# Performance work log

Measured on AMD Instinct MI355X. Metric: run time of the kernel, lower is better.

The kernel has to match this reference:

```python
import jax, jax.numpy as jnp
from jax import lax
import numpy as np

M_FILTERS = 128   # rows of responses D
N_CHANNELS = 1024 # cols of responses D (spectral channels)
BATCH = 4096
N_LAYERS = 17
IMAX = 50


def setup_inputs() -> dict:
    key = jax.random.key(0)
    k1, k2, k3, k4 = jax.random.split(key, 4)
    t1 = jax.random.normal(k1, (BATCH, N_CHANNELS), dtype=jnp.float32)
    t2 = jax.random.normal(k2, (BATCH, N_CHANNELS), dtype=jnp.float32)
    params = jax.random.uniform(k3, (M_FILTERS, N_LAYERS), dtype=jnp.float32)
    responses = jax.random.normal(k4, (M_FILTERS, N_CHANNELS), dtype=jnp.float32)
    return {
        "t1": t1,
        "t2": t2,
        "params": params,
        "thick_min": jnp.float32(0.0),
        "thick_max": jnp.float32(1.0),
        "beta_range": jnp.float32(0.1),
        "responses": responses,
    }


def _coherence_reduce(D0):
    """Faithful vectorized version of the 50-iteration coherence-reduction loop.

    The original per-row Python loop (Ri[i] > Rth branch) only reads row i and
    pre-computed Rth/delta, so it is exactly a masked row update.
    torch.linalg.eig on the symmetric matrices G is replaced by eigh (same
    eigenpairs up to sign/order; order is fixed by the explicit descending sort,
    and only the top-M eigenpairs reach the output D[:M,:]).
    """
    Mr, Nr = D0.shape
    ratio = jnp.float32(Nr / Mr)
    eye_b = jnp.eye(Nr, dtype=bool)

    def body(_, D):
        D = D / jnp.linalg.norm(D)                      # Frobenius norm over (0,1)
        G = D.T @ D                                     # [N, N]
        Sigma, V = jnp.linalg.eigh(G)
        Sigma = jnp.where(jnp.abs(Sigma) > 1e-10, ratio, Sigma)
        G = (V * Sigma[None, :]) @ V.T                  # V diag(Sigma) V^T
        G0 = jnp.abs(G - jnp.diag(jnp.diag(G)))
        Ri = jnp.sum(G0, axis=0)                        # [N]
        Rth = jnp.min(Ri)
        delta = Rth / (Nr - 1)
        mask = (Ri > Rth)[:, None]                      # rows to clip
        Gn = jnp.where(mask, delta * jnp.sign(G), G)
        Gn = jnp.where(eye_b, G, Gn)                    # keep original diagonal
        G = (Gn + Gn.T) * 0.5
        Sigma, V = jnp.linalg.eigh(G)
        order = jnp.argsort(-Sigma)                     # descending
        Sigma = Sigma[order]
        V = V[:, order]
        # Original: Sigma[M:-1]=0 then D = diag(Sigma)^{1/2} @ V.T, D = D[:M,:].
        # Only the top-M eigenpairs contribute to the first M rows.
        Dn = jnp.power(Sigma[:Mr], 0.5)[:, None] * V[:, :Mr].T  # [M, N]
        return Dn

    return lax.fori_loop(0, IMAX, body, D0)


def reference(t1, t2, params, thick_min, thick_max, beta_range, responses):
    # HybnetLoss: MSE match loss + hinge range loss (filter_loss is zeroed in source)
    match_loss = jnp.mean((t1 - t2) ** 2)
    d = jnp.float32(0.01)
    res = jnp.maximum((params - thick_min - d) / (-d),
                      (params - thick_max + d) / d)
    range_loss = jnp.mean(jnp.maximum(res, jnp.zeros_like(res)))
    original_loss = match_loss + beta_range * range_loss

    # HybnetLoss_plus: coherence-reduction regularizer on the response matrix
    D = _coherence_reduce(responses)
    rloss = jnp.mean((D - responses) ** 2)
    return original_loss + rloss
```

## Files before the change

kernel.cpp:

```cpp
#include <hip/hip_runtime.h>

#define NBLK 256
#define NTHR 512

#define OFF_G    0
#define OFF_QT   1048576
#define OFF_Y    1179648
#define OFF_C    1703936
#define OFF_RP   1851392
#define OFF_ACC  1867776
#define OFF_BAR  1867792

#define BAR_A 0
#define BAR_B 64
#define BAR_C 128
#define BAR_E 136

typedef float v4f __attribute__((ext_vector_type(4)));

__device__ __forceinline__ void cld4_8(v4f& a, v4f& b, v4f& c, v4f& d,
                                       v4f& e, v4f& f, v4f& g, v4f& h,
                                       const float* pa, const float* pb,
                                       const float* pc, const float* pd,
                                       const float* pe, const float* pf,
                                       const float* pg, const float* ph) {
    asm volatile("global_load_dwordx4 %0, %8, off sc1\n\t"
                 "global_load_dwordx4 %1, %9, off sc1\n\t"
                 "global_load_dwordx4 %2, %10, off sc1\n\t"
                 "global_load_dwordx4 %3, %11, off sc1\n\t"
                 "global_load_dwordx4 %4, %12, off sc1\n\t"
                 "global_load_dwordx4 %5, %13, off sc1\n\t"
                 "global_load_dwordx4 %6, %14, off sc1\n\t"
                 "global_load_dwordx4 %7, %15, off sc1\n\t"
                 "s_waitcnt vmcnt(0)"
                 : "=&v"(a), "=&v"(b), "=&v"(c), "=&v"(d),
                   "=&v"(e), "=&v"(f), "=&v"(g), "=&v"(h)
                 : "v"(pa), "v"(pb), "v"(pc), "v"(pd),
                   "v"(pe), "v"(pf), "v"(pg), "v"(ph) : "memory");
}
__device__ __forceinline__ void cld4_4(v4f& a, v4f& b, v4f& c, v4f& d,
                                       const float* pa, const float* pb,
                                       const float* pc, const float* pd) {
    asm volatile("global_load_dwordx4 %0, %4, off sc1\n\t"
                 "global_load_dwordx4 %1, %5, off sc1\n\t"
                 "global_load_dwordx4 %2, %6, off sc1\n\t"
                 "global_load_dwordx4 %3, %7, off sc1\n\t"
                 "s_waitcnt vmcnt(0)"
                 : "=&v"(a), "=&v"(b), "=&v"(c), "=&v"(d)
                 : "v"(pa), "v"(pb), "v"(pc), "v"(pd) : "memory");
}
__device__ __forceinline__ void cld4_2(v4f& a, v4f& b,
                                       const float* pa, const float* pb) {
    asm volatile("global_load_dwordx4 %0, %2, off sc1\n\t"
                 "global_load_dwordx4 %1, %3, off sc1\n\t"
                 "s_waitcnt vmcnt(0)"
                 : "=&v"(a), "=&v"(b) : "v"(pa), "v"(pb) : "memory");
}
__device__ __forceinline__ void cld1_4(float& a, float& b, float& c, float& d,
                                       const float* pa, const float* pb,
                                       const float* pc, const float* pd) {
    asm volatile("global_load_dword %0, %4, off sc1\n\t"
                 "global_load_dword %1, %5, off sc1\n\t"
                 "global_load_dword %2, %6, off sc1\n\t"
                 "global_load_dword %3, %7, off sc1\n\t"
                 "s_waitcnt vmcnt(0)"
                 : "=&v"(a), "=&v"(b), "=&v"(c), "=&v"(d)
                 : "v"(pa), "v"(pb), "v"(pc), "v"(pd) : "memory");
}
__device__ __forceinline__ void cld1_8(float& a, float& b, float& c, float& d,
                                       float& e, float& f, float& g, float& h,
                                       const float* pa, const float* pb,
                                       const float* pc, const float* pd,
                                       const float* pe, const float* pf,
                                       const float* pg, const float* ph) {
    asm volatile("global_load_dword %0, %8, off sc1\n\t"
                 "global_load_dword %1, %9, off sc1\n\t"
                 "global_load_dword %2, %10, off sc1\n\t"
                 "global_load_dword %3, %11, off sc1\n\t"
                 "global_load_dword %4, %12, off sc1\n\t"
                 "global_load_dword %5, %13, off sc1\n\t"
                 "global_load_dword %6, %14, off sc1\n\t"
                 "global_load_dword %7, %15, off sc1\n\t"
                 "s_waitcnt vmcnt(0)"
                 : "=&v"(a), "=&v"(b), "=&v"(c), "=&v"(d),
                   "=&v"(e), "=&v"(f), "=&v"(g), "=&v"(h)
                 : "v"(pa), "v"(pb), "v"(pc), "v"(pd),
                   "v"(pe), "v"(pf), "v"(pg), "v"(ph) : "memory");
}
__device__ __forceinline__ void iss2(v4f& a, v4f& b,
                                     const float* pa, const float* pb) {
    asm volatile("global_load_dwordx4 %0, %2, off sc1\n\t"
                 "global_load_dwordx4 %1, %3, off sc1"
                 : "=&v"(a), "=&v"(b) : "v"(pa), "v"(pb) : "memory");
}
__device__ __forceinline__ void wt2(v4f& a, v4f& b) {
    asm volatile("s_waitcnt vmcnt(0)"
                 : "+v"(a), "+v"(b) :: "memory");
}
__device__ __forceinline__ void iss1(v4f& a, const float* pa) {
    asm volatile("global_load_dwordx4 %0, %1, off sc1"
                 : "=&v"(a) : "v"(pa) : "memory");
}
__device__ __forceinline__ void wt1(v4f& a) {
    asm volatile("s_waitcnt vmcnt(0)" : "+v"(a) :: "memory");
}

__device__ __forceinline__ void syncL() {
    asm volatile("s_waitcnt lgkmcnt(0)" ::: "memory");
    __builtin_amdgcn_s_barrier();
    asm volatile("" ::: "memory");
}

__device__ __forceinline__ void ast2(float* p, float a, float b) {
    union { unsigned long long u; float f[2]; } c; c.f[0] = a; c.f[1] = b;
    __hip_atomic_store((unsigned long long*)p, c.u,
                       __ATOMIC_RELAXED, __HIP_MEMORY_SCOPE_AGENT);
}
__device__ __forceinline__ float ald(const float* p) {
    return __hip_atomic_load(p, __ATOMIC_RELAXED, __HIP_MEMORY_SCOPE_AGENT);
}
__device__ __forceinline__ void ast(float* p, float x) {
    __hip_atomic_store(p, x, __ATOMIC_RELAXED, __HIP_MEMORY_SCOPE_AGENT);
}

__device__ __forceinline__ void bar_arrive(unsigned* bb, int line) {
    __syncthreads();
    if (threadIdx.x == 0)
        __hip_atomic_fetch_add(bb + line * 16, 1u,
                               __ATOMIC_RELAXED, __HIP_MEMORY_SCOPE_AGENT);
}
__device__ __forceinline__ void bar_wait(unsigned* bb, int wbase, int nlines,
                                         unsigned tgt) {
    if ((int)threadIdx.x < nlines) {
        while (__hip_atomic_load(bb + (wbase + threadIdx.x) * 16,
                                 __ATOMIC_RELAXED, __HIP_MEMORY_SCOPE_AGENT) < tgt)
            __builtin_amdgcn_s_sleep(1);
    }
    __builtin_amdgcn_s_waitcnt(0);
    __syncthreads();
}

union Smem {
    struct { float As[32][68]; float Bs[32][68]; float Rs[64][17]; } gg;
    struct { float Cs[128][129]; float inv_d[16]; float irs[128];
             float Xs[16][64]; } chol;
    struct { float Ri[1024]; float red[512]; float As[32][36]; float Bs[32][68]; } gy;
    struct { float As[32][68]; float Bs[32][68]; float red[512]; } tb;
    float red[512];
};

__device__ __forceinline__ void dev_match(Smem* sm, const float* t1, const float* t2,
                                          float* accb, int w) {
    int tid = threadIdx.x;
    const float4* a = (const float4*)t1;
    const float4* b = (const float4*)t2;
    float s = 0.f;
    for (int i = w * 512 + tid; i < 1048576; i += 218 * 512) {
        float4 x = a[i], y = b[i];
        float d0 = x.x - y.x, d1 = x.y - y.y, d2 = x.z - y.z, d3 = x.w - y.w;
        s += d0 * d0 + d1 * d1 + d2 * d2 + d3 * d3;
    }
    sm->red[tid] = s; __syncthreads();
    for (int w2 = 256; w2 > 0; w2 >>= 1) {
        if (tid < w2) sm->red[tid] += sm->red[tid + w2];
        __syncthreads();
    }
    if (tid == 0) atomicAdd(&accb[0], sm->red[0]);
    __syncthreads();
}

__device__ __forceinline__ void dev_range(Smem* sm, const float* params, const float* tmin,
                                          const float* tmax, float* accb) {
    int tid = threadIdx.x;
    float a = tmin[0], b = tmax[0];
    const float d = 0.01f;
    float s = 0.f;
    for (int i = tid; i < 128 * 17; i += 512) {
        float p = params[i];
        float r1 = (p - a - d) / (-d);
        float r2 = (p - b + d) / d;
        s += fmaxf(fmaxf(r1, r2), 0.f);
    }
    sm->red[tid] = s; __syncthreads();
    for (int w = 256; w > 0; w >>= 1) {
        if (tid < w) sm->red[tid] += sm->red[tid + w];
        __syncthreads();
    }
    if (tid == 0) atomicAdd(&accb[1], sm->red[0]);
    __syncthreads();
}

__device__ __forceinline__ void dev_sumsq(Smem* sm, const float* X, float* accb, int w) {
    int tid = threadIdx.x;
    float s = 0.f;
    for (int i = w * 512 + tid; i < 131072; i += 2048) { float v = X[i]; s += v * v; }
    sm->red[tid] = s; __syncthreads();
    for (int w2 = 256; w2 > 0; w2 >>= 1) {
        if (tid < w2) sm->red[tid] += sm->red[tid + w2];
        __syncthreads();
    }
    if (tid == 0) atomicAdd(&accb[3], sm->red[0]);
    __syncthreads();
}

__device__ __forceinline__ void dev_syrk(Smem* sm, const float* A, const float* B,
                                         float* C, int bid) {
    int tid = threadIdx.x;
    int q0 = (bid & 1) * 64, p0 = ((bid >> 1) & 1) * 64, z = bid >> 2;
    int kc0 = z * 128;
    int p = tid & 63, kg = (tid >> 6) * 4;
    int tx = tid & 15, ty = tid >> 4;
    float acc[2][4] = {};
    v4f av, bv;
    iss2(av, bv, &A[(p0 + p) * 1024 + kc0 + kg], &B[(q0 + p) * 1024 + kc0 + kg]);
    for (int ck = 0; ck < 4; ++ck) {
        wt2(av, bv);
        sm->gg.As[kg + 0][p] = av.x; sm->gg.As[kg + 1][p] = av.y;
        sm->gg.As[kg + 2][p] = av.z; sm->gg.As[kg + 3][p] = av.w;
        sm->gg.Bs[kg + 0][p] = bv.x; sm->gg.Bs[kg + 1][p] = bv.y;
        sm->gg.Bs[kg + 2][p] = bv.z; sm->gg.Bs[kg + 3][p] = bv.w;
        syncL();
        if (ck < 3) {
            int kn = kc0 + (ck + 1) * 32 + kg;
            iss2(av, bv, &A[(p0 + p) * 1024 + kn], &B[(q0 + p) * 1024 + kn]);
        }
        for (int k = 0; k < 32; ++k) {
            float2 a2 = *(const float2*)&sm->gg.As[k][ty * 2];
            float4 b4 = *(const float4*)&sm->gg.Bs[k][tx * 4];
            acc[0][0] += a2.x * b4.x; acc[0][1] += a2.x * b4.y;
            acc[0][2] += a2.x * b4.z; acc[0][3] += a2.x * b4.w;
            acc[1][0] += a2.y * b4.x; acc[1][1] += a2.y * b4.y;
            acc[1][2] += a2.y * b4.z; acc[1][3] += a2.y * b4.w;
        }
        syncL();
    }
    #pragma unroll
    for (int i = 0; i < 2; ++i)
        #pragma unroll
        for (int j = 0; j < 4; ++j)
            atomicAdd(&C[(p0 + ty * 2 + i) * 128 + q0 + tx * 4 + j], acc[i][j]);
}

__device__ __forceinline__ void dev_cholTrsm(Smem* sm, const float* C, const float* RHS,
                                             float* Qt, int bid) {
    int tid = threadIdx.x;
    {
        const float* base = C + tid * 32;
        v4f z0, z1, z2, z3, z4, z5, z6, z7;
        cld4_8(z0, z1, z2, z3, z4, z5, z6, z7,
               base, base + 4, base + 8, base + 12,
               base + 16, base + 20, base + 24, base + 28);
        int r = tid >> 2, c0 = (tid & 3) * 32;
        *(v4f*)&sm->chol.Cs[r][c0]      = z0; *(v4f*)&sm->chol.Cs[r][c0 + 4]  = z1;
        *(v4f*)&sm->chol.Cs[r][c0 + 8]  = z2; *(v4f*)&sm->chol.Cs[r][c0 + 12] = z3;
        *(v4f*)&sm->chol.Cs[r][c0 + 16] = z4; *(v4f*)&sm->chol.Cs[r][c0 + 20] = z5;
        *(v4f*)&sm->chol.Cs[r][c0 + 24] = z6; *(v4f*)&sm->chol.Cs[r][c0 + 28] = z7;
    }
    __syncthreads();
    int lane = tid & 63;
    for (int kb = 0; kb < 8; ++kb) {
        int k0 = kb * 16;
        if (tid < 64) {
            float P0[16], P1[16], invs[16];
            #pragma unroll
            for (int u = 0; u < 16; ++u) {
                P0[u] = sm->chol.Cs[lane][k0 + u];
                P1[u] = sm->chol.Cs[lane + 64][k0 + u];
            }
            #pragma unroll
            for (int kk = 0; kk < 16; ++kk) {
                int k = k0 + kk;
                int src = k & 63;
                bool hi = (k >= 64);
                float pr[16];
                #pragma unroll
                for (int u = 0; u < 16; ++u)
                    if (u >= kk) pr[u] = __shfl(hi ? P1[u] : P0[u], src);
                float inv = __builtin_amdgcn_rcpf(pr[kk]);
                invs[kk] = inv;
                float f0 = (lane > k) ? P0[kk] * inv : 0.f;
                float f1 = ((lane + 64) > k) ? P1[kk] * inv : 0.f;
                #pragma unroll
                for (int u = kk + 1; u < 16; ++u) {
                    P0[u] -= f0 * pr[u];
                    P1[u] -= f1 * pr[u];
                }
            }
            #pragma unroll
            for (int u = 0; u < 16; ++u) {
                sm->chol.Cs[lane][k0 + u] = P0[u];
                sm->chol.Cs[lane + 64][k0 + u] = P1[u];
            }
            if (lane == 0) {
                #pragma unroll
                for (int kk = 0; kk < 16; ++kk) sm->chol.inv_d[kk] = invs[kk];
            }
        }
        __syncthreads();
        int base = k0 + 16;
        if (base < 128) {
            int hh = tid >> 6, cc = tid & 63;
            int j1 = base + cc;
            int j2 = base + cc + 64;
            bool has1 = (j1 < 128), has2 = (j2 < 128);
            float w1[16], w2[16];
            if (has1) {
                #pragma unroll
                for (int u = 0; u < 16; ++u) w1[u] = sm->chol.Cs[j1][k0 + u] * sm->chol.inv_d[u];
            }
            if (has2) {
                #pragma unroll
                for (int u = 0; u < 16; ++u) w2[u] = sm->chol.Cs[j2][k0 + u] * sm->chol.inv_d[u];
            }
            int rlo = hh * 16;
            int istart = rlo > base ? rlo : base;
            for (int i = istart; i < rlo + 16; ++i) {
                float v[16];
                #pragma unroll
                for (int u = 0; u < 16; ++u) v[u] = sm->chol.Cs[i][k0 + u];
                float a1 = 0.f, a2 = 0.f;
                #pragma unroll
                for (int u = 0; u < 16; ++u) { a1 += v[u] * w1[u]; a2 += v[u] * w2[u]; }
                if (has1) sm->chol.Cs[i][j1] -= a1;
                if (has2) sm->chol.Cs[i][j2] -= a2;
            }
        }
        __syncthreads();
    }
    if (tid < 128) sm->chol.irs[tid] = __builtin_amdgcn_rsqf(sm->chol.Cs[tid][tid]);
    int c = tid & 63, h = tid >> 6;
    int j0 = bid * 64;
    float acc[16];
    {
        const float* p = &RHS[(h * 16) * 1024 + j0 + c];
        cld1_8(acc[0], acc[1], acc[2], acc[3], acc[4], acc[5], acc[6], acc[7],
               p, p + 1024, p + 2048, p + 3072, p + 4096, p + 5120, p + 6144, p + 7168);
        cld1_8(acc[8], acc[9], acc[10], acc[11], acc[12], acc[13], acc[14], acc[15],
               p + 8192, p + 9216, p + 10240, p + 11264,
               p + 12288, p + 13312, p + 14336, p + 15360);
    }
    __syncthreads();
    for (int pb = 0; pb < 8; ++pb) {
        int p0 = pb * 16;
        if (h == pb) {
            #pragma unroll
            for (int kk = 0; kk < 16; ++kk) {
                int k = p0 + kk;
                float irsk = sm->chol.irs[k];
                float x = acc[kk] * irsk;
                acc[kk] = x;
                sm->chol.Xs[kk][c] = x;
                float xs = x * irsk;
                #pragma unroll
                for (int r = kk + 1; r < 16; ++r)
                    acc[r] -= sm->chol.Cs[p0 + r][k] * xs;
            }
        }
        __syncthreads();
        if (h > pb) {
            int rb = h * 16;
            #pragma unroll
            for (int kk = 0; kk < 16; ++kk) {
                int k = p0 + kk;
                float xs = sm->chol.Xs[kk][c] * sm->chol.irs[k];
                #pragma unroll
                for (int r = 0; r < 16; ++r)
                    acc[r] -= sm->chol.Cs[rb + r][k] * xs;
            }
        }
        __syncthreads();
    }
    #pragma unroll
    for (int r = 0; r < 16; ++r)
        ast(&Qt[(h * 16 + r) * 1024 + j0 + c], acc[r]);
}

__device__ __forceinline__ void dev_gemmG(Smem* sm, const float* Qt, float* G,
                                          float* Rpart, int bid) {
    int tid = threadIdx.x;
    int tx = tid & 15, ty = tid >> 4;
    int bx = bid & 15, by = bid >> 4;
    int a0 = by * 64, b0 = bx * 64;
    int r0 = tid >> 4, c4 = (tid & 15) << 2;
    float acc[2][4] = {};
    v4f av, bv;
    iss2(av, bv, &Qt[r0 * 1024 + a0 + c4], &Qt[r0 * 1024 + b0 + c4]);
    for (int kc = 0; kc < 128; kc += 32) {
        wt2(av, bv);
        *(v4f*)&sm->gg.As[r0][c4] = av;
        *(v4f*)&sm->gg.Bs[r0][c4] = bv;
        syncL();
        if (kc < 96) {
            int kn = kc + 32;
            iss2(av, bv, &Qt[(kn + r0) * 1024 + a0 + c4],
                 &Qt[(kn + r0) * 1024 + b0 + c4]);
        }
        for (int k = 0; k < 32; ++k) {
            float2 a2 = *(const float2*)&sm->gg.As[k][ty * 2];
            float4 b4 = *(const float4*)&sm->gg.Bs[k][tx * 4];
            acc[0][0] += a2.x * b4.x; acc[0][1] += a2.x * b4.y;
            acc[0][2] += a2.x * b4.z; acc[0][3] += a2.x * b4.w;
            acc[1][0] += a2.y * b4.x; acc[1][1] += a2.y * b4.y;
            acc[1][2] += a2.y * b4.z; acc[1][3] += a2.y * b4.w;
        }
        syncL();
    }
    float rsum[2] = {0.f, 0.f};
    #pragma unroll
    for (int i = 0; i < 2; ++i) {
        int aa = a0 + ty * 2 + i;
        float g[4];
        #pragma unroll
        for (int j = 0; j < 4; ++j) g[j] = 8.f * acc[i][j];
        float* gp = &G[aa * 1024 + b0 + tx * 4];
        ast2(gp, g[0], g[1]);
        ast2(gp + 2, g[2], g[3]);
        int bb = b0 + tx * 4;
        #pragma unroll
        for (int j = 0; j < 4; ++j) rsum[i] += (aa == bb + j) ? 0.f : fabsf(g[j]);
    }
    sm->gg.Rs[ty * 2 + 0][tx] = rsum[0];
    sm->gg.Rs[ty * 2 + 1][tx] = rsum[1];
    __syncthreads();
    if (tid < 64) {
        float s = 0.f;
        #pragma unroll
        for (int x = 0; x < 16; ++x) s += sm->gg.Rs[tid][x];
        ast(&Rpart[(a0 + tid) * 16 + bx], s);
    }
}

__device__ __forceinline__ void dev_ri(Smem* sm, const float* Rpart,
                                       float* rth, float* delta) {
    int tid = threadIdx.x;
    int e0 = tid, e1 = tid + 512;
    v4f t0, t1, t2, t3, u0, u1, u2, u3;
    cld4_8(t0, t1, t2, t3, u0, u1, u2, u3,
           &Rpart[e0 * 16], &Rpart[e0 * 16 + 4],
           &Rpart[e0 * 16 + 8], &Rpart[e0 * 16 + 12],
           &Rpart[e1 * 16], &Rpart[e1 * 16 + 4],
           &Rpart[e1 * 16 + 8], &Rpart[e1 * 16 + 12]);
    float s0 = 0.f;
    s0 += t0.x; s0 += t0.y; s0 += t0.z; s0 += t0.w;
    s0 += t1.x; s0 += t1.y; s0 += t1.z; s0 += t1.w;
    s0 += t2.x; s0 += t2.y; s0 += t2.z; s0 += t2.w;
    s0 += t3.x; s0 += t3.y; s0 += t3.z; s0 += t3.w;
    float s1 = 0.f;
    s1 += u0.x; s1 += u0.y; s1 += u0.z; s1 += u0.w;
    s1 += u1.x; s1 += u1.y; s1 += u1.z; s1 += u1.w;
    s1 += u2.x; s1 += u2.y; s1 += u2.z; s1 += u2.w;
    s1 += u3.x; s1 += u3.y; s1 += u3.z; s1 += u3.w;
    sm->gy.Ri[e0] = s0;
    sm->gy.Ri[e1] = s1;
    float mn = fminf(s0, s1);
    #pragma unroll
    for (int off = 32; off > 0; off >>= 1)
        mn = fminf(mn, __shfl_xor(mn, off));
    if ((tid & 63) == 0) sm->gy.red[tid >> 6] = mn;
    __syncthreads();
    float r = sm->gy.red[0];
    #pragma unroll
    for (int w = 1; w < 8; ++w) r = fminf(r, sm->gy.red[w]);
    *rth = r;
    *delta = r / 1023.f;
}

__device__ __forceinline__ void dev_gemmY(Smem* sm, const float* Qt, const float* G,
                                          float rth, float delta, float* Y, int bid) {
    int tid = threadIdx.x;
    int j0 = (bid & 15) * 64;
    int m0 = ((bid >> 4) & 3) * 32;
    int kz = bid >> 6;
    int kc0 = kz * 256;
    int tx = tid & 15, ty = tid >> 4;
    int m = (tid & 255) >> 3, k4 = (tid & 7) << 2;
    int rg = tid >> 4, cg = (tid & 15) << 2;
    float acc[4] = {};
    v4f q, g0;
    if (tid < 256) iss1(q, &Qt[(m0 + m) * 1024 + kc0 + k4]);
    iss1(g0, &G[(kc0 + rg) * 1024 + j0 + cg]);
    for (int kc = kc0; kc < kc0 + 256; kc += 32) {
        wt1(g0);
        if (tid < 256) {
            wt1(q);
            *(v4f*)&sm->gy.As[m][k4] = q;
        }
        {
            int a = kc + rg;
            float ria = sm->gy.Ri[a];
            v4f bw;
            #pragma unroll
            for (int u = 0; u < 4; ++u) {
                int b = j0 + cg + u;
                float g = g0[u];
                float sg = delta * ((g > 0.f) ? 1.f : ((g < 0.f) ? -1.f : 0.f));
                float ga = (ria > rth) ? sg : g;
                float gb = (sm->gy.Ri[b] > rth) ? sg : g;
                bw[u] = (a == b) ? g : 0.5f * (ga + gb);
            }
            *(v4f*)&sm->gy.Bs[rg][cg] = bw;
        }
        syncL();
        if (kc < kc0 + 224) {
            int kn = kc + 32;
            if (tid < 256) iss1(q, &Qt[(m0 + m) * 1024 + kn + k4]);
            iss1(g0, &G[(kn + rg) * 1024 + j0 + cg]);
        }
        #pragma unroll
        for (int kb = 0; kb < 8; ++kb) {
            v4f qa = *(const v4f*)&sm->gy.As[ty][kb * 4];
            #pragma unroll
            for (int kk = 0; kk < 4; ++kk) {
                float4 b4 = *(const float4*)&sm->gy.Bs[kb * 4 + kk][tx * 4];
                float a = qa[kk];
                acc[0] += a * b4.x; acc[1] += a * b4.y;
                acc[2] += a * b4.z; acc[3] += a * b4.w;
            }
        }
        syncL();
    }
    #pragma unroll
    for (int j = 0; j < 4; ++j)
        atomicAdd(&Y[(m0 + ty) * 1024 + j0 + tx * 4 + j], acc[j]);
}

__device__ __forceinline__ void dev_trB(Smem* sm, const float* Qt, const float* G,
                                        const float* Rpart, float* accb, int bid) {
    int tid = threadIdx.x;
    float rth, delta;
    dev_ri(sm, Rpart, &rth, &delta);
    __syncthreads();
    int tx = tid & 15, ty = tid >> 4;
    int a0 = (bid >> 4) * 64, b0 = (bid & 15) * 64;
    int r0 = tid >> 4, c4 = (tid & 15) << 2;
    float acc[2][4] = {};
    for (int kc = 0; kc < 128; kc += 32) {
        v4f av, bv;
        cld4_2(av, bv, &Qt[(kc + r0) * 1024 + a0 + c4],
               &Qt[(kc + r0) * 1024 + b0 + c4]);
        *(v4f*)&sm->tb.As[r0][c4] = av;
        *(v4f*)&sm->tb.Bs[r0][c4] = bv;
        __syncthreads();
        for (int k = 0; k < 32; ++k) {
            float2 a2 = *(const float2*)&sm->tb.As[k][ty * 2];
            float4 b4 = *(const float4*)&sm->tb.Bs[k][tx * 4];
            acc[0][0] += a2.x * b4.x; acc[0][1] += a2.x * b4.y;
            acc[0][2] += a2.x * b4.z; acc[0][3] += a2.x * b4.w;
            acc[1][0] += a2.y * b4.x; acc[1][1] += a2.y * b4.y;
            acc[1][2] += a2.y * b4.z; acc[1][3] += a2.y * b4.w;
        }
        __syncthreads();
    }
    float rib[4];
    #pragma unroll
    for (int j = 0; j < 4; ++j) {
        int bb = b0 + tx * 4 + j;
        v4f t0, t1, t2, t3;
        cld4_4(t0, t1, t2, t3, &Rpart[bb * 16], &Rpart[bb * 16 + 4],
               &Rpart[bb * 16 + 8], &Rpart[bb * 16 + 12]);
        float s = 0.f;
        s += t0.x; s += t0.y; s += t0.z; s += t0.w;
        s += t1.x; s += t1.y; s += t1.z; s += t1.w;
        s += t2.x; s += t2.y; s += t2.z; s += t2.w;
        s += t3.x; s += t3.y; s += t3.z; s += t3.w;
        rib[j] = s;
    }
    float s = 0.f;
    #pragma unroll
    for (int i = 0; i < 2; ++i) {
        int aa = a0 + ty * 2 + i;
        v4f t0, t1, t2, t3;
        cld4_4(t0, t1, t2, t3, &Rpart[aa * 16], &Rpart[aa * 16 + 4],
               &Rpart[aa * 16 + 8], &Rpart[aa * 16 + 12]);
        float ria = 0.f;
        ria += t0.x; ria += t0.y; ria += t0.z; ria += t0.w;
        ria += t1.x; ria += t1.y; ria += t1.z; ria += t1.w;
        ria += t2.x; ria += t2.y; ria += t2.z; ria += t2.w;
        ria += t3.x; ria += t3.y; ria += t3.z; ria += t3.w;
        float g0, g1, g2, g3;
        const float* gp = &G[aa * 1024 + b0 + tx * 4];
        cld1_4(g0, g1, g2, g3, gp, gp + 1, gp + 2, gp + 3);
        float gv[4] = {g0, g1, g2, g3};
        #pragma unroll
        for (int j = 0; j < 4; ++j) {
            int bb = b0 + tx * 4 + j;
            float g = gv[j];
            float sg = delta * ((g > 0.f) ? 1.f : ((g < 0.f) ? -1.f : 0.f));
            float ga = (ria > rth) ? sg : g;
            float gb = (rib[j] > rth) ? sg : g;
            float gp2 = (aa == bb) ? g : 0.5f * (ga + gb);
            s += gp2 * acc[i][j];
        }
    }
    __syncthreads();
    sm->tb.red[tid] = s;
    __syncthreads();
    for (int w = 256; w > 0; w >>= 1) {
        if (tid < w) sm->tb.red[tid] += sm->tb.red[tid + w];
        __syncthreads();
    }
    if (tid == 0) atomicAdd(&accb[2], sm->tb.red[0]);
}

__global__ __launch_bounds__(512) void mega(const float* __restrict__ t1,
                                            const float* __restrict__ t2,
                                            const float* __restrict__ params,
                                            const float* __restrict__ tmin,
                                            const float* __restrict__ tmax,
                                            const float* __restrict__ beta,
                                            const float* __restrict__ R,
                                            float* ws, float* out) {
    float* G     = ws + OFF_G;
    float* Qt    = ws + OFF_QT;
    float* Y     = ws + OFF_Y;
    float* C     = ws + OFF_C;
    float* Rpart = ws + OFF_RP;
    float* accb  = ws + OFF_ACC;
    unsigned* bb = (unsigned*)(ws + OFF_BAR);
    __shared__ Smem sm;
    int bid = blockIdx.x;
    int tid = threadIdx.x;
    unsigned phA = 0, phB = 0, phC = 0, phE = 0;

    if (bid < 32) {
        ast(&C[bid * 512 + tid], 0.f);
    } else if (bid < 250) dev_match(&sm, t1, t2, accb, bid - 32);
    else if (bid == 250) dev_range(&sm, params, tmin, tmax, accb);
    else if (bid < 255) dev_sumsq(&sm, R, accb, bid - 251);
    ++phC;
    if (bid < 32) {
        bar_arrive(bb, BAR_C + (bid >> 2));
        bar_wait(bb, BAR_C, 8, phC * 4);
        dev_syrk(&sm, R, R, C, bid);
    }
    ++phC;
    if (bid < 32) bar_arrive(bb, BAR_C + (bid >> 2));
    if (bid < 16) {
        bar_wait(bb, BAR_C, 8, phC * 4);
        dev_cholTrsm(&sm, C, R, Qt, bid);
    }
    ++phE;
    if (bid < 16) bar_arrive(bb, BAR_E + (bid >> 2));
    bar_wait(bb, BAR_E, 4, phE * 4);

    for (int it = 0; it < 50; ++it) {
        dev_gemmG(&sm, Qt, G, Rpart, bid);
        ast(&Y[bid * 512 + tid], 0.f);
        if (bid < 32) ast(&C[bid * 512 + tid], 0.f);
        ++phA;
        bar_arrive(bb, BAR_A + (bid & 63));
        bar_wait(bb, BAR_A, 64, phA * 4);
        {
            float rth, delta;
            dev_ri(&sm, Rpart, &rth, &delta);
            dev_gemmY(&sm, Qt, G, rth, delta, Y, bid);
        }
        ++phB;
        bar_arrive(bb, BAR_B + (bid & 63));
        if (bid < 32) {
            bar_wait(bb, BAR_B, 64, phB * 4);
            dev_syrk(&sm, Y, Y, C, bid);
        }
        ++phC;
        if (bid < 32) bar_arrive(bb, BAR_C + (bid >> 2));
        if (bid < 16) {
            bar_wait(bb, BAR_C, 8, phC * 4);
            dev_cholTrsm(&sm, C, Y, Qt, bid);
        }
        ++phE;
        if (bid < 16) bar_arrive(bb, BAR_E + (bid >> 2));
        bar_wait(bb, BAR_E, 4, phE * 4);
    }

    dev_trB(&sm, Qt, G, Rpart, accb, bid);
    ++phA;
    bar_arrive(bb, BAR_A + (bid & 63));
    if (bid == 0) {
        bar_wait(bb, BAR_A, 64, phA * 4);
        if (tid == 0)
            out[0] = ald(&accb[0]) / 4194304.f + beta[0] * (ald(&accb[1]) / 2176.f)
                   + (ald(&accb[2]) + ald(&accb[3])) / 131072.f;
    }
}

extern "C" void kernel_launch(void* const* d_in, const int* in_sizes, int n_in,
                              void* d_out, int out_size, void* d_ws, size_t ws_size,
                              hipStream_t stream) {
    const float* t1 = (const float*)d_in[0];
    const float* t2 = (const float*)d_in[1];
    const float* params = (const float*)d_in[2];
    const float* tmin = (const float*)d_in[3];
    const float* tmax = (const float*)d_in[4];
    const float* beta = (const float*)d_in[5];
    const float* R = (const float*)d_in[6];
    float* ws = (float*)d_ws;
    float* out = (float*)d_out;

    hipMemsetAsync(ws + OFF_ACC, 0, 9280, stream);
    mega<<<NBLK, NTHR, 0, stream>>>(t1, t2, params, tmin, tmax, beta, R, ws, out);
}
```

Baseline: 7.202 ms.

## Replace atomic Y accumulation with split-K partial buffers reduced inside SYRK

gemmY now writes each K-slice's partial result to its own buffer with plain vector stores, instead of doing atomicAdd into a Y that had to be zeroed every iteration. The SYRK stage sums the four partials while loading them, and writes the reduced Y to a separate buffer (YS) that the Cholesky/TRSM stage reads. The G stores in gemmG become dwordx4 stores followed by a wait, replacing pairs of 64-bit atomic stores. This removes the per-iteration atomics and the Y zeroing, but SYRK now reads four times as much data and adds extra stores.

```diff
diff --git a/kernel.cpp b/kernel.cpp
--- a/kernel.cpp
+++ b/kernel.cpp
@@ -7,6 +7,7 @@
 #define OFF_QT   1048576
 #define OFF_Y    1179648
 #define OFF_C    1703936
+#define OFF_YS   1720320
 #define OFF_RP   1851392
 #define OFF_ACC  1867776
 #define OFF_BAR  1867792
@@ -104,6 +105,23 @@
 __device__ __forceinline__ void wt1(v4f& a) {
     asm volatile("s_waitcnt vmcnt(0)" : "+v"(a) :: "memory");
 }
+__device__ __forceinline__ void wt8_0(v4f& a, v4f& b, v4f& c, v4f& d,
+                                      v4f& e, v4f& f, v4f& g, v4f& h) {
+    asm volatile("s_waitcnt vmcnt(0)"
+                 : "+v"(a), "+v"(b), "+v"(c), "+v"(d),
+                   "+v"(e), "+v"(f), "+v"(g), "+v"(h) :: "memory");
+}
+__device__ __forceinline__ void st4w(float* p, v4f v) {
+    asm volatile("global_store_dwordx4 %0, %1, off sc0 sc1\n\t"
+                 "s_waitcnt vmcnt(0)"
+                 :: "v"(p), "v"(v) : "memory");
+}
+__device__ __forceinline__ void st4_2w(float* p0, v4f v0, float* p1, v4f v1) {
+    asm volatile("global_store_dwordx4 %0, %1, off sc0 sc1\n\t"
+                 "global_store_dwordx4 %2, %3, off sc0 sc1\n\t"
+                 "s_waitcnt vmcnt(0)"
+                 :: "v"(p0), "v"(v0), "v"(p1), "v"(v1) : "memory");
+}
 
 __device__ __forceinline__ void syncL() {
     asm volatile("s_waitcnt lgkmcnt(0)" ::: "memory");
@@ -241,6 +259,64 @@
             atomicAdd(&C[(p0 + ty * 2 + i) * 128 + q0 + tx * 4 + j], acc[i][j]);
 }
 
+__device__ __forceinline__ void dev_syrkY(Smem* sm, const float* Yp, float* C,
+                                          float* YS, int bid) {
+    int tid = threadIdx.x;
+    int q0 = (bid & 1) * 64, p0 = ((bid >> 1) & 1) * 64, z = bid >> 2;
+    int kc0 = z * 128;
+    int p = tid & 63, kg = (tid >> 6) * 4;
+    int tx = tid & 15, ty = tid >> 4;
+    bool wq = (bid & 1) == 0;
+    float acc[2][4] = {};
+    v4f a0, a1, a2, a3, b0, b1, b2, b3;
+    {
+        const float* pa = &Yp[(p0 + p) * 1024 + kc0 + kg];
+        const float* pb = &Yp[(q0 + p) * 1024 + kc0 + kg];
+        iss2(a0, b0, pa, pb);
+        iss2(a1, b1, pa + 131072, pb + 131072);
+        iss2(a2, b2, pa + 262144, pb + 262144);
+        iss2(a3, b3, pa + 393216, pb + 393216);
+    }
+    for (int ck = 0; ck < 4; ++ck) {
+        wt8_0(a0, a1, a2, a3, b0, b1, b2, b3);
+        v4f av = a0 + a1 + a2 + a3;
+        v4f bv = b0 + b1 + b2 + b3;
+        if (wq) {
+            float* ys = &YS[(p0 + p) * 1024 + kc0 + ck * 32 + kg];
+            ast2(ys, av.x, av.y);
+            ast2(ys + 2, av.z, av.w);
+        }
+        sm->gg.As[kg + 0][p] = av.x; sm->gg.As[kg + 1][p] = av.y;
+        sm->gg.As[kg + 2][p] = av.z; sm->gg.As[kg + 3][p] = av.w;
+        sm->gg.Bs[kg + 0][p] = bv.x; sm->gg.Bs[kg + 1][p] = bv.y;
+        sm->gg.Bs[kg + 2][p] = bv.z; sm->gg.Bs[kg + 3][p] = bv.w;
+        syncL();
+        if (ck < 3) {
+            int kn = kc0 + (ck + 1) * 32 + kg;
+            const float* pa = &Yp[(p0 + p) * 1024 + kn];
+            const float* pb = &Yp[(q0 + p) * 1024 + kn];
+            iss2(a0, b0, pa, pb);
+            iss2(a1, b1, pa + 131072, pb + 131072);
+            iss2(a2, b2, pa + 262144, pb + 262144);
+            iss2(a3, b3, pa + 393216, pb + 393216);
+        }
+        for (int k = 0; k < 32; ++k) {
+            float2 a2r = *(const float2*)&sm->gg.As[k][ty * 2];
+            float4 b4 = *(const float4*)&sm->gg.Bs[k][tx * 4];
+            acc[0][0] += a2r.x * b4.x; acc[0][1] += a2r.x * b4.y;
+            acc[0][2] += a2r.x * b4.z; acc[0][3] += a2r.x * b4.w;
+            acc[1][0] += a2r.y * b4.x; acc[1][1] += a2r.y * b4.y;
+            acc[1][2] += a2r.y * b4.z; acc[1][3] += a2r.y * b4.w;
+        }
+        syncL();
+    }
+    #pragma unroll
+    for (int i = 0; i < 2; ++i)
+        #pragma unroll
+        for (int j = 0; j < 4; ++j)
+            atomicAdd(&C[(p0 + ty * 2 + i) * 128 + q0 + tx * 4 + j], acc[i][j]);
+}
+
 __device__ __forceinline__ void dev_cholTrsm(Smem* sm, const float* C, const float* RHS,
                                              float* Qt, int bid) {
     int tid = threadIdx.x;
@@ -405,19 +481,17 @@
         }
         syncL();
     }
+    int aa0 = a0 + ty * 2, aa1 = aa0 + 1;
+    v4f gv0, gv1;
+    #pragma unroll
+    for (int j = 0; j < 4; ++j) { gv0[j] = 8.f * acc[0][j]; gv1[j] = 8.f * acc[1][j]; }
+    st4_2w(&G[aa0 * 1024 + b0 + tx * 4], gv0, &G[aa1 * 1024 + b0 + tx * 4], gv1);
     float rsum[2] = {0.f, 0.f};
-    #pragma unroll
-    for (int i = 0; i < 2; ++i) {
-        int aa = a0 + ty * 2 + i;
-        float g[4];
-        #pragma unroll
-        for (int j = 0; j < 4; ++j) g[j] = 8.f * acc[i][j];
-        float* gp = &G[aa * 1024 + b0 + tx * 4];
-        ast2(gp, g[0], g[1]);
-        ast2(gp + 2, g[2], g[3]);
-        int bb = b0 + tx * 4;
-        #pragma unroll
-        for (int j = 0; j < 4; ++j) rsum[i] += (aa == bb + j) ? 0.f : fabsf(g[j]);
+    int bb0 = b0 + tx * 4;
+    #pragma unroll
+    for (int j = 0; j < 4; ++j) {
+        rsum[0] += (aa0 == bb0 + j) ? 0.f : fabsf(gv0[j]);
+        rsum[1] += (aa1 == bb0 + j) ? 0.f : fabsf(gv1[j]);
     }
     sm->gg.Rs[ty * 2 + 0][tx] = rsum[0];
     sm->gg.Rs[ty * 2 + 1][tx] = rsum[1];
@@ -466,7 +540,7 @@
 }
 
 __device__ __forceinline__ void dev_gemmY(Smem* sm, const float* Qt, const float* G,
-                                          float rth, float delta, float* Y, int bid) {
+                                          float rth, float delta, float* Yp, int bid) {
     int tid = threadIdx.x;
     int j0 = (bid & 15) * 64;
     int m0 = ((bid >> 4) & 3) * 32;
@@ -519,9 +593,8 @@
         }
         syncL();
     }
-    #pragma unroll
-    for (int j = 0; j < 4; ++j)
-        atomicAdd(&Y[(m0 + ty) * 1024 + j0 + tx * 4 + j], acc[j]);
+    v4f accv = {acc[0], acc[1], acc[2], acc[3]};
+    st4w(&Yp[kz * 131072 + (m0 + ty) * 1024 + j0 + tx * 4], accv);
 }
 
 __device__ __forceinline__ void dev_trB(Smem* sm, const float* Qt, const float* G,
@@ -612,8 +685,9 @@
                                             float* ws, float* out) {
     float* G     = ws + OFF_G;
     float* Qt    = ws + OFF_QT;
-    float* Y     = ws + OFF_Y;
+    float* Yp    = ws + OFF_Y;
     float* C     = ws + OFF_C;
+    float* YS    = ws + OFF_YS;
     float* Rpart = ws + OFF_RP;
     float* accb  = ws + OFF_ACC;
     unsigned* bb = (unsigned*)(ws + OFF_BAR);
@@ -645,7 +719,6 @@
 
     for (int it = 0; it < 50; ++it) {
         dev_gemmG(&sm, Qt, G, Rpart, bid);
-        ast(&Y[bid * 512 + tid], 0.f);
         if (bid < 32) ast(&C[bid * 512 + tid], 0.f);
         ++phA;
         bar_arrive(bb, BAR_A + (bid & 63));
@@ -653,19 +726,19 @@
         {
             float rth, delta;
             dev_ri(&sm, Rpart, &rth, &delta);
-            dev_gemmY(&sm, Qt, G, rth, delta, Y, bid);
+            dev_gemmY(&sm, Qt, G, rth, delta, Yp, bid);
         }
         ++phB;
         bar_arrive(bb, BAR_B + (bid & 63));
         if (bid < 32) {
             bar_wait(bb, BAR_B, 64, phB * 4);
-            dev_syrk(&sm, Y, Y, C, bid);
+            dev_syrkY(&sm, Yp, C, YS, bid);
         }
         ++phC;
         if (bid < 32) bar_arrive(bb, BAR_C + (bid >> 2));
         if (bid < 16) {
             bar_wait(bb, BAR_C, 8, phC * 4);
-            dev_cholTrsm(&sm, C, Y, Qt, bid);
+            dev_cholTrsm(&sm, C, YS, Qt, bid);
         }
         ++phE;
         if (bid < 16) bar_arrive(bb, BAR_E + (bid >> 2));
```

New measurement: 7.527 ms. 1.05x slower.
